# Performance work log

Measured on AMD Instinct MI355X. Metric: run time of the kernel, lower is better.

The kernel has to match this reference:

```python
import jax, jax.numpy as jnp
import numpy as np

N = 100000
E = 1600000
IN_DIM = 128
HID = 64
CLS = 10
L = 3
EPS = 1e-5


def setup_inputs() -> dict:
    key = jax.random.key(0)
    ks = jax.random.split(key, 12)
    x = jax.random.normal(ks[0], (N, IN_DIM), dtype=jnp.float32)
    edge_index = jax.random.randint(ks[1], (2, E), 0, N, dtype=jnp.int64)
    s = lambda k, shape, fan: jax.random.normal(k, shape, dtype=jnp.float32) / np.sqrt(fan)
    return {
        "x": x,
        "edge_index": edge_index,
        "fc1_w": s(ks[2], (HID, IN_DIM), IN_DIM),
        "fc1_b": jnp.zeros((HID,), jnp.float32),
        "lin_l_w": s(ks[3], (L, HID, HID), HID),   # neighbor (aggregated) weight, with bias
        "lin_l_b": jnp.zeros((L, HID), jnp.float32),
        "lin_r_w": s(ks[4], (L, HID, HID), HID),   # root/self weight, no bias (PyG SAGEConv)
        "bn_gamma": jnp.ones((L, HID), jnp.float32),
        "bn_beta": jnp.zeros((L, HID), jnp.float32),
        "fc2_w": s(ks[5], (CLS, HID), HID),
        "fc2_b": jnp.zeros((CLS,), jnp.float32),
    }


def reference(x, edge_index, fc1_w, fc1_b, lin_l_w, lin_l_b, lin_r_w,
              bn_gamma, bn_beta, fc2_w, fc2_b):
    src, dst = edge_index[0], edge_index[1]
    # in-degree counts for mean aggregation (zero-degree nodes -> 0 output)
    deg = jax.ops.segment_sum(jnp.ones((E,), x.dtype), dst, num_segments=N)
    inv_deg = jnp.where(deg > 0, 1.0 / jnp.maximum(deg, 1.0), 0.0)[:, None]

    h = jax.nn.relu(x @ fc1_w.T + fc1_b)  # [N, HID]
    for l in range(L):
        # SAGEConv: mean-aggregate neighbor features, then lin_l(agg) + lin_r(self)
        agg = jax.ops.segment_sum(h[src], dst, num_segments=N) * inv_deg  # [N, HID]
        h = agg @ lin_l_w[l].T + lin_l_b[l] + h @ lin_r_w[l].T
        # batch norm over node dimension (training batch statistics)
        mu = jnp.mean(h, axis=0)
        var = jnp.mean(jnp.square(h - mu), axis=0)
        h = (h - mu) * jax.lax.rsqrt(var + EPS) * bn_gamma[l] + bn_beta[l]
        h = jax.nn.relu(h)
    logits = h @ fc2_w.T + fc2_b  # [N, CLS]
    return jax.nn.log_softmax(logits, axis=1)
```

## Files before the change

kernel.cpp:

```cpp
#include <hip/hip_runtime.h>

#define N_NODES 100000
#define N_EDGES 1600000
#define IN_DIM  128
#define HID     64
#define CLS     10
#define NLAYER  3
#define BN_EPS  1e-5f
#define INV_N   (1.0f / N_NODES)
#define SREP    8
#define CAP     40
#define NW      32
#define WNODES  (N_NODES / NW)
#define PBLK    512
#define EPB     (N_EDGES / PBLK)
#define BCAP    152

typedef __attribute__((ext_vector_type(8))) short bf16x8;
typedef __attribute__((ext_vector_type(4))) float f32x4;
typedef __attribute__((ext_vector_type(2))) float f32x2;

__device__ __forceinline__ int clampi(int v, int lo, int hi) {
    return v < lo ? lo : (v > hi ? hi : v);
}

__device__ __forceinline__ unsigned bf16rne(float v) {
    unsigned u = __float_as_uint(v);
    return (u + 0x7fffu + ((u >> 16) & 1u)) >> 16;
}

__device__ __forceinline__ float bf2f(unsigned short u) {
    return __uint_as_float((unsigned)u << 16);
}

__device__ __forceinline__ void splitbf(float v, unsigned short& hi, unsigned short& lo) {
    unsigned h = bf16rne(v);
    hi = (unsigned short)h;
    lo = (unsigned short)bf16rne(v - __uint_as_float(h << 16));
}

#if defined(__has_builtin)
# if __has_builtin(__builtin_amdgcn_cvt_pk_f32_fp8) && __has_builtin(__builtin_amdgcn_cvt_pk_fp8_f32)
#  define HW_FP8 1
# endif
#endif
#ifndef HW_FP8
# define HW_FP8 0
#endif

__device__ __forceinline__ void fp8dec4(unsigned u, float* o) {
#if HW_FP8
    f32x2 lo = __builtin_amdgcn_cvt_pk_f32_fp8((int)u, false);
    f32x2 hi = __builtin_amdgcn_cvt_pk_f32_fp8((int)u, true);
    o[0] = lo[0]; o[1] = lo[1]; o[2] = hi[0]; o[3] = hi[1];
#else
#pragma unroll
    for (int k = 0; k < 4; k++) {
        unsigned b = (u >> (8 * k)) & 0xffu;
        unsigned s = b >> 7, e = (b >> 3) & 15u, m = b & 7u;
        float v = e ? __uint_as_float(((e + 120u) << 23) | (m << 20)) : (float)m * 0x1p-9f;
        o[k] = s ? -v : v;
    }
#endif
}

__device__ __forceinline__ unsigned fp8enc1(float v) {
#if HW_FP8
    return (unsigned)__builtin_amdgcn_cvt_pk_fp8_f32(v, 0.f, 0, false) & 0xffu;
#else
    float a = fabsf(v);
    unsigned s = __float_as_uint(v) >> 31;
    if (a > 448.f) a = 448.f;
    unsigned r;
    if (a < 0x1p-6f) {
        r = (unsigned)__float2int_rn(a * 512.f);
    } else {
        unsigned u = __float_as_uint(a);
        int ex = (int)(u >> 23) - 127;
        unsigned man = u & 0x7fffffu;
        unsigned mr = (man + 0x7ffffu + ((man >> 20) & 1u)) >> 20;
        if (mr == 8u) { mr = 0; ex++; }
        if (ex > 8) { ex = 8; mr = 7; }
        r = ((unsigned)(ex + 7) << 3) | mr;
    }
    return (s << 7) | r;
#endif
}

__device__ __forceinline__ float stat_sum(const float* __restrict__ s, int idx) {
    float a = 0.f;
#pragma unroll
    for (int r = 0; r < SREP; r++) a += s[r * 2 * HID + idx];
    return a;
}

__global__ __launch_bounds__(256) void k_bin(const int* __restrict__ ei,
                                             unsigned* __restrict__ binned,
                                             int* __restrict__ bcnt) {
    __shared__ int lcnt[NW];
    int t = threadIdx.x, b = blockIdx.x;
    if (t < NW) lcnt[t] = 0;
    __syncthreads();
    int e0 = b * EPB;
    int e1 = e0 + EPB; if (e1 > N_EDGES) e1 = N_EDGES;
    for (int e = e0 + t; e < e1; e += 256) {
        int d = clampi(ei[N_EDGES + e], 0, N_NODES - 1);
        int s = clampi(ei[e],           0, N_NODES - 1);
        int w  = d / WNODES;
        int dw = d - w * WNODES;
        int j = atomicAdd(&lcnt[w], 1);
        if (j < BCAP)
            binned[((size_t)w * PBLK + b) * BCAP + j] = ((unsigned)dw << 17) | (unsigned)s;
    }
    __syncthreads();
    if (t < NW) bcnt[t * PBLK + b] = lcnt[t] < BCAP ? lcnt[t] : BCAP;
}

__global__ __launch_bounds__(256) void k_scat2(const unsigned* __restrict__ binned,
                                               const int* __restrict__ bcnt,
                                               int* __restrict__ cursor,
                                               int* __restrict__ ssrc) {
    int w  = blockIdx.x >> 3;
    int jb = blockIdx.x & 7;
    int wv = threadIdx.x >> 6, ln = threadIdx.x & 63;
    for (int b = jb * 4 + wv; b < PBLK; b += 32) {
        int cnt = bcnt[w * PBLK + b];
        const unsigned* run = &binned[((size_t)w * PBLK + b) * BCAP];
        for (int i = ln; i < cnt; i += 64) {
            unsigned pk = run[i];
            int s  = (int)(pk & 0x1ffffu);
            int d  = w * WNODES + (int)(pk >> 17);
            int j = atomicAdd(&cursor[d], 1);
            if (j < CAP) ssrc[(size_t)d * CAP + j] = s;
        }
    }
}

__global__ void k_wprep(const float* __restrict__ lw, const float* __restrict__ rw,
                        short* __restrict__ whi, short* __restrict__ wlo) {
    int i = blockIdx.x * 256 + threadIdx.x;
    if (i >= NLAYER * 2 * HID * HID) return;
    int l   = i / (2 * HID * HID);
    int rem = i % (2 * HID * HID);
    int op  = rem / (HID * HID);
    int jk  = rem % (HID * HID);
    float w = (op == 0) ? lw[(size_t)l * HID * HID + jk] : rw[(size_t)l * HID * HID + jk];
    unsigned short h_, l_;
    splitbf(w, h_, l_);
    whi[i] = (short)h_;
    wlo[i] = (short)l_;
}

__global__ void k_wprep1(const float* __restrict__ w1,
                         short* __restrict__ w1hi, short* __restrict__ w1lo) {
    int i = blockIdx.x * 256 + threadIdx.x;
    if (i >= HID * IN_DIM) return;
    unsigned short h_, l_;
    splitbf(w1[i], h_, l_);
    w1hi[i] = (short)h_;
    w1lo[i] = (short)l_;
}

__global__ void k_wprep2(const float* __restrict__ w2,
                         short* __restrict__ w2hi, short* __restrict__ w2lo) {
    int i = blockIdx.x * 256 + threadIdx.x;
    if (i >= 16 * HID) return;
    int j = i >> 6, k = i & 63;
    float w = (j < CLS) ? w2[(size_t)j * HID + k] : 0.f;
    unsigned short h_, l_;
    splitbf(w, h_, l_);
    w2hi[i] = (short)h_;
    w2lo[i] = (short)l_;
}

__global__ __launch_bounds__(128) void k_fc1_mfma(const float* __restrict__ x,
                                                  const short* __restrict__ w1hi,
                                                  const short* __restrict__ w1lo,
                                                  const float* __restrict__ b,
                                                  short* __restrict__ hbf,
                                                  unsigned char* __restrict__ hf8) {
    int t = threadIdx.x;
    int lane = t & 63;
    int wv = t >> 6;
    int lr = lane & 15;
    int kg = lane >> 4;
    int n0 = (blockIdx.x * 2 + wv) * 16;

    f32x4 acc0 = {0.f,0.f,0.f,0.f}, acc1 = {0.f,0.f,0.f,0.f};
    f32x4 acc2 = {0.f,0.f,0.f,0.f}, acc3 = {0.f,0.f,0.f,0.f};

#pragma unroll
    for (int kh = 0; kh < 4; kh++) {
        int kb = kg * 8 + kh * 32;
        const float4 a01 = *(const float4*)&x[(size_t)(n0 + lr) * IN_DIM + kb];
        const float4 a23 = *(const float4*)&x[(size_t)(n0 + lr) * IN_DIM + kb + 4];
        float av[8] = {a01.x,a01.y,a01.z,a01.w,a23.x,a23.y,a23.z,a23.w};
        bf16x8 ah, al;
#pragma unroll
        for (int e = 0; e < 8; e++) {
            unsigned h1 = bf16rne(av[e]);
            ah[e] = (short)h1;
            al[e] = (short)bf16rne(av[e] - __uint_as_float(h1 << 16));
        }
#define JT1(JT_, ACC_) { \
        const bf16x8 fwh = *(const bf16x8*)&w1hi[(size_t)(JT_ * 16 + lr) * IN_DIM + kb]; \
        const bf16x8 fwl = *(const bf16x8*)&w1lo[(size_t)(JT_ * 16 + lr) * IN_DIM + kb]; \
        ACC_ = __builtin_amdgcn_mfma_f32_16x16x32_bf16(ah, fwh, ACC_, 0, 0, 0); \
        ACC_ = __builtin_amdgcn_mfma_f32_16x16x32_bf16(ah, fwl, ACC_, 0, 0, 0); \
        ACC_ = __builtin_amdgcn_mfma_f32_16x16x32_bf16(al, fwh, ACC_, 0, 0, 0); \
    }
        JT1(0, acc0) JT1(1, acc1) JT1(2, acc2) JT1(3, acc3)
#undef JT1
    }

    float bv0 = b[lr], bv1 = b[16 + lr], bv2 = b[32 + lr], bv3 = b[48 + lr];
#define EPI1(JT_, ACC_, BV_) { \
        _Pragma("unroll") \
        for (int r = 0; r < 4; r++) { \
            float v = fmaxf(ACC_[r] + BV_, 0.f); \
            size_t idx = (size_t)(n0 + kg * 4 + r) * HID + JT_ * 16 + lr; \
            hbf[idx] = (short)bf16rne(v); \
            hf8[idx] = (unsigned char)fp8enc1(v); \
        } \
    }
    EPI1(0, acc0, bv0) EPI1(1, acc1, bv1) EPI1(2, acc2, bv2) EPI1(3, acc3, bv3)
#undef EPI1
}

__global__ __launch_bounds__(256, 6) void k_agg(const unsigned char* __restrict__ act_f8,
                                                const int* __restrict__ cursor,
                                                const int* __restrict__ ssrc,
                                                short* __restrict__ agg_bf) {
    int wave = (blockIdx.x * 256 + threadIdx.x) >> 6;
    int lane = threadIdx.x & 63;
    int g  = lane >> 4;
    int gl = lane & 15;
    int n = wave;
    if (n >= N_NODES) return;

    int cnt = cursor[n];
    cnt = cnt < CAP ? cnt : CAP;
    int s = n * CAP;
    int e = s + cnt;
    float ax = 0.f, ay = 0.f, az = 0.f, aw = 0.f;
    int i = s + g;

#define ACCP(P_) do { \
        float v_[4]; \
        fp8dec4(P_, v_); \
        ax += v_[0]; ay += v_[1]; az += v_[2]; aw += v_[3]; \
    } while (0)

    for (; i + 12 < e; i += 16) {
        int u0 = ssrc[i], u1 = ssrc[i + 4], u2 = ssrc[i + 8], u3 = ssrc[i + 12];
        unsigned p0 = *(const unsigned*)&act_f8[(size_t)u0 * HID + gl * 4];
        unsigned p1 = *(const unsigned*)&act_f8[(size_t)u1 * HID + gl * 4];
        unsigned p2 = *(const unsigned*)&act_f8[(size_t)u2 * HID + gl * 4];
        unsigned p3 = *(const unsigned*)&act_f8[(size_t)u3 * HID + gl * 4];
        ACCP(p0); ACCP(p1); ACCP(p2); ACCP(p3);
    }
    for (; i < e; i += 4) {
        int u = ssrc[i];
        unsigned pv = *(const unsigned*)&act_f8[(size_t)u * HID + gl * 4];
        ACCP(pv);
    }
#undef ACCP

#pragma unroll
    for (int st = 16; st <= 32; st <<= 1) {
        ax += __shfl_xor(ax, st);
        ay += __shfl_xor(ay, st);
        az += __shfl_xor(az, st);
        aw += __shfl_xor(aw, st);
    }
    if (g == 0) {
        float id = (cnt > 0) ? 1.0f / (float)cnt : 0.f;
        ushort4 r;
        r.x = (unsigned short)bf16rne(ax * id);
        r.y = (unsigned short)bf16rne(ay * id);
        r.z = (unsigned short)bf16rne(az * id);
        r.w = (unsigned short)bf16rne(aw * id);
        *(ushort4*)&agg_bf[(size_t)n * HID + gl * 4] = r;
    }
}

__global__ __launch_bounds__(128) void k_gemm_mfma(
    short* __restrict__ agg,
    const short* __restrict__ hs,
    const float* __restrict__ scp, const float* __restrict__ shp, int use_bn,
    const short* __restrict__ wlhi, const short* __restrict__ wllo,
    const short* __restrict__ wrhi, const short* __restrict__ wrlo,
    const float* __restrict__ lb, float* __restrict__ stats_out)
{
    __shared__ float lstat[2 * HID];
    int t = threadIdx.x;
    for (int i = t; i < 2 * HID; i += 128) lstat[i] = 0.f;
    __syncthreads();
    int lane = t & 63;
    int wv = t >> 6;
    int lr = lane & 15;
    int kg = lane >> 4;
    int n0 = (blockIdx.x * 2 + wv) * 16;

    f32x4 acc0 = {0.f,0.f,0.f,0.f}, acc1 = {0.f,0.f,0.f,0.f};
    f32x4 acc2 = {0.f,0.f,0.f,0.f}, acc3 = {0.f,0.f,0.f,0.f};

#pragma unroll
    for (int kh = 0; kh < 2; kh++) {
        int kb = kg * 8 + kh * 32;
        bf16x8 ah = *(const bf16x8*)&agg[(size_t)(n0 + lr) * HID + kb];
        bf16x8 bh = *(const bf16x8*)&hs[(size_t)(n0 + lr) * HID + kb];
        if (use_bn) {
#pragma unroll
            for (int e = 0; e < 8; e++) {
                int c = kb + e;
                float v = fmaxf(bf2f((unsigned short)bh[e]) * scp[c] + shp[c], 0.f);
                bh[e] = (short)bf16rne(v);
            }
        }
#define JT(JT_, ACC_) { \
        const bf16x8 fwlh = *(const bf16x8*)&wlhi[(size_t)(JT_ * 16 + lr) * HID + kb]; \
        const bf16x8 fwll = *(const bf16x8*)&wllo[(size_t)(JT_ * 16 + lr) * HID + kb]; \
        const bf16x8 fwrh = *(const bf16x8*)&wrhi[(size_t)(JT_ * 16 + lr) * HID + kb]; \
        const bf16x8 fwrl = *(const bf16x8*)&wrlo[(size_t)(JT_ * 16 + lr) * HID + kb]; \
        ACC_ = __builtin_amdgcn_mfma_f32_16x16x32_bf16(ah, fwlh, ACC_, 0, 0, 0); \
        ACC_ = __builtin_amdgcn_mfma_f32_16x16x32_bf16(ah, fwll, ACC_, 0, 0, 0); \
        ACC_ = __builtin_amdgcn_mfma_f32_16x16x32_bf16(bh, fwrh, ACC_, 0, 0, 0); \
        ACC_ = __builtin_amdgcn_mfma_f32_16x16x32_bf16(bh, fwrl, ACC_, 0, 0, 0); \
    }
        JT(0, acc0) JT(1, acc1) JT(2, acc2) JT(3, acc3)
#undef JT
    }

    float lbv0 = lb[lr], lbv1 = lb[16 + lr], lbv2 = lb[32 + lr], lbv3 = lb[48 + lr];
#define EPI(JT_, ACC_, LBV_) { \
        float s_ = 0.f, q_ = 0.f; \
        _Pragma("unroll") \
        for (int r = 0; r < 4; r++) { \
            float v = ACC_[r] + LBV_; \
            size_t idx = (size_t)(n0 + kg * 4 + r) * HID + JT_ * 16 + lr; \
            agg[idx] = (short)bf16rne(v); \
            s_ += v; q_ += v * v; \
        } \
        s_ += __shfl_xor(s_, 16); s_ += __shfl_xor(s_, 32); \
        q_ += __shfl_xor(q_, 16); q_ += __shfl_xor(q_, 32); \
        if (kg == 0) { \
            atomicAdd(&lstat[JT_ * 16 + lr], s_); \
            atomicAdd(&lstat[HID + JT_ * 16 + lr], q_); \
        } \
    }
    EPI(0, acc0, lbv0) EPI(1, acc1, lbv1) EPI(2, acc2, lbv2) EPI(3, acc3, lbv3)
#undef EPI
    __syncthreads();
    int rep = blockIdx.x & (SREP - 1);
    for (int i = t; i < 2 * HID; i += 128)
        atomicAdd(&stats_out[rep * 2 * HID + i], lstat[i]);
}

__global__ __launch_bounds__(256) void k_bnact(const float* __restrict__ stats,
                                               const float* __restrict__ gamma,
                                               const float* __restrict__ beta,
                                               const short* __restrict__ pre_bf,
                                               unsigned char* __restrict__ act_f8,
                                               float* __restrict__ scO,
                                               float* __restrict__ shO) {
    __shared__ float lsc[HID], lsh[HID];
    int t = threadIdx.x;
    if (t < HID) {
        float mu  = stat_sum(stats, t) * INV_N;
        float var = stat_sum(stats, HID + t) * INV_N - mu * mu;
        float s = gamma[t] * rsqrtf(var + BN_EPS);
        lsc[t] = s;
        lsh[t] = beta[t] - mu * s;
        if (blockIdx.x == 0) { scO[t] = s; shO[t] = lsh[t]; }
    }
    __syncthreads();
    int gl = t & 15;
    float4 s4 = *(const float4*)&lsc[gl * 4];
    float4 h4 = *(const float4*)&lsh[gl * 4];
    size_t idx = (size_t)blockIdx.x * 256 + t;
    size_t total = (size_t)N_NODES * HID / 4;
    size_t stride = (size_t)gridDim.x * 256;
    for (; idx < total; idx += stride) {
        ushort4 v = ((const ushort4*)pre_bf)[idx];
        float f0 = fmaxf(bf2f(v.x) * s4.x + h4.x, 0.f);
        float f1 = fmaxf(bf2f(v.y) * s4.y + h4.y, 0.f);
        float f2 = fmaxf(bf2f(v.z) * s4.z + h4.z, 0.f);
        float f3 = fmaxf(bf2f(v.w) * s4.w + h4.w, 0.f);
        unsigned pk = fp8enc1(f0) | (fp8enc1(f1) << 8) | (fp8enc1(f2) << 16) | (fp8enc1(f3) << 24);
        ((unsigned*)act_f8)[idx] = pk;
    }
}

__global__ void k_bnprep(const float* __restrict__ stats,
                         const float* __restrict__ gamma,
                         const float* __restrict__ beta,
                         float* __restrict__ sc, float* __restrict__ sh) {
    int t = threadIdx.x;
    float mu  = stat_sum(stats, t) * INV_N;
    float var = stat_sum(stats, HID + t) * INV_N - mu * mu;
    float s = gamma[t] * rsqrtf(var + BN_EPS);
    sc[t] = s;
    sh[t] = beta[t] - mu * s;
}

__global__ __launch_bounds__(128) void k_fc2_mfma(const short* __restrict__ h_bf,
                                                  const float* __restrict__ scp,
                                                  const float* __restrict__ shp,
                                                  const short* __restrict__ w2hi,
                                                  const short* __restrict__ w2lo,
                                                  const float* __restrict__ b2,
                                                  float* __restrict__ out) {
    int t = threadIdx.x;
    int lane = t & 63;
    int wv = t >> 6;
    int lr = lane & 15;
    int kg = lane >> 4;
    int n0 = (blockIdx.x * 2 + wv) * 16;

    f32x4 acc = {0.f,0.f,0.f,0.f};
#pragma unroll
    for (int kh = 0; kh < 2; kh++) {
        int kb = kg * 8 + kh * 32;
        bf16x8 ah = *(const bf16x8*)&h_bf[(size_t)(n0 + lr) * HID + kb];
#pragma unroll
        for (int e = 0; e < 8; e++) {
            int c = kb + e;
            float v = fmaxf(bf2f((unsigned short)ah[e]) * scp[c] + shp[c], 0.f);
            ah[e] = (short)bf16rne(v);
        }
        const bf16x8 wh = *(const bf16x8*)&w2hi[(size_t)lr * HID + kb];
        const bf16x8 wl = *(const bf16x8*)&w2lo[(size_t)lr * HID + kb];
        acc = __builtin_amdgcn_mfma_f32_16x16x32_bf16(ah, wh, acc, 0, 0, 0);
        acc = __builtin_amdgcn_mfma_f32_16x16x32_bf16(ah, wl, acc, 0, 0, 0);
    }
    float b2v = (lr < CLS) ? b2[lr] : 0.f;
#pragma unroll
    for (int r = 0; r < 4; r++) {
        int row = n0 + kg * 4 + r;
        float v = (lr < CLS) ? (acc[r] + b2v) : -3.4e38f;
        float m = v;
#pragma unroll
        for (int o = 1; o < 16; o <<= 1) m = fmaxf(m, __shfl_xor(m, o));
        float ev = (lr < CLS) ? __expf(v - m) : 0.f;
        float se = ev;
#pragma unroll
        for (int o = 1; o < 16; o <<= 1) se += __shfl_xor(se, o);
        float lse = m + __logf(se);
        if (lr < CLS) out[(size_t)row * CLS + lr] = v - lse;
    }
}

extern "C" void kernel_launch(void* const* d_in, const int* in_sizes, int n_in,
                              void* d_out, int out_size, void* d_ws, size_t ws_size,
                              hipStream_t stream) {
    const float* x        = (const float*)d_in[0];
    const int*   ei       = (const int*)d_in[1];
    const float* fc1_w    = (const float*)d_in[2];
    const float* fc1_b    = (const float*)d_in[3];
    const float* lin_l_w  = (const float*)d_in[4];
    const float* lin_l_b  = (const float*)d_in[5];
    const float* lin_r_w  = (const float*)d_in[6];
    const float* bn_gamma = (const float*)d_in[7];
    const float* bn_beta  = (const float*)d_in[8];
    const float* fc2_w    = (const float*)d_in[9];
    const float* fc2_b    = (const float*)d_in[10];
    float* out = (float*)d_out;

    char* p = (char*)d_ws;
    short*         hA  = (short*)p;         p += (size_t)N_NODES * HID * 2;
    short*         hB  = (short*)p;         p += (size_t)N_NODES * HID * 2;
    unsigned char* f0  = (unsigned char*)p; p += (size_t)N_NODES * HID;
    char*  zbase   = p;
    int*   cursor  = (int*)p;   p += (size_t)N_NODES * 4;
    float* stats   = (float*)p; p += (size_t)NLAYER * SREP * 2 * HID * 4;
    size_t zbytes  = (size_t)(p - zbase);
    int*      ssrc   = (int*)p;      p += (size_t)N_NODES * CAP * 4;
    unsigned* binned = (unsigned*)p; p += (size_t)NW * PBLK * BCAP * 4;
    int*      bcnt   = (int*)p;      p += (size_t)NW * PBLK * 4;
    short* whi     = (short*)p; p += (size_t)NLAYER * 2 * HID * HID * 2;
    short* wlo     = (short*)p; p += (size_t)NLAYER * 2 * HID * HID * 2;
    short* w1hi    = (short*)p; p += (size_t)HID * IN_DIM * 2;
    short* w1lo    = (short*)p; p += (size_t)HID * IN_DIM * 2;
    short* w2hi    = (short*)p; p += (size_t)16 * HID * 2;
    short* w2lo    = (short*)p; p += (size_t)16 * HID * 2;
    float* scbuf   = (float*)p; p += (size_t)NLAYER * HID * 4;
    float* shbuf   = (float*)p; p += (size_t)NLAYER * HID * 4;

    hipMemsetAsync(zbase, 0, zbytes, stream);
    k_wprep  <<<(NLAYER * 2 * HID * HID + 255) / 256, 256, 0, stream>>>(lin_l_w, lin_r_w, whi, wlo);
    k_wprep1 <<<(HID * IN_DIM + 255) / 256, 256, 0, stream>>>(fc1_w, w1hi, w1lo);
    k_wprep2 <<<(16 * HID + 255) / 256, 256, 0, stream>>>(fc2_w, w2hi, w2lo);
    k_bin    <<<PBLK, 256, 0, stream>>>(ei, binned, bcnt);
    k_scat2  <<<NW * 8, 256, 0, stream>>>(binned, bcnt, cursor, ssrc);
    k_fc1_mfma<<<3125, 128, 0, stream>>>(x, w1hi, w1lo, fc1_b, hA, f0);

    const int AGG_GRID = (N_NODES + 3) / 4;

    short* hin = hA;
    short* buf = hB;
    for (int l = 0; l < NLAYER; l++) {
        int use_bn = (l > 0);
        const float* sc_in = scbuf + (size_t)(l > 0 ? l - 1 : 0) * HID;
        const float* sh_in = shbuf + (size_t)(l > 0 ? l - 1 : 0) * HID;
        k_agg<<<AGG_GRID, 256, 0, stream>>>(f0, cursor, ssrc, buf);
        k_gemm_mfma<<<3125, 128, 0, stream>>>(buf, hin,
                                              sc_in, sh_in, use_bn,
                                              whi + (size_t)(l * 2 + 0) * HID * HID,
                                              wlo + (size_t)(l * 2 + 0) * HID * HID,
                                              whi + (size_t)(l * 2 + 1) * HID * HID,
                                              wlo + (size_t)(l * 2 + 1) * HID * HID,
                                              lin_l_b + (size_t)l * HID,
                                              stats + (size_t)l * SREP * 2 * HID);
        if (l < NLAYER - 1) {
            k_bnact<<<1024, 256, 0, stream>>>(stats + (size_t)l * SREP * 2 * HID,
                                              bn_gamma + (size_t)l * HID,
                                              bn_beta + (size_t)l * HID,
                                              buf, f0,
                                              scbuf + (size_t)l * HID,
                                              shbuf + (size_t)l * HID);
        } else {
            k_bnprep<<<1, 64, 0, stream>>>(stats + (size_t)l * SREP * 2 * HID,
                                           bn_gamma + (size_t)l * HID,
                                           bn_beta + (size_t)l * HID,
                                           scbuf + (size_t)l * HID,
                                           shbuf + (size_t)l * HID);
        }
        short* th = hin; hin = buf; buf = th;
    }
    k_fc2_mfma<<<3125, 128, 0, stream>>>(hin, scbuf + (size_t)2 * HID, shbuf + (size_t)2 * HID,
                                         w2hi, w2lo, fc2_b, out);
}
```

Before: 371.9 us.

## Build per-node neighbor lists in LDS per bin and stream them out coalesced

The edge binning now uses 128 destination bins of 782 nodes each, and the per-bin scatter kernel runs one block per bin. Each block builds the neighbor slot lists and counts in shared memory with LDS atomics, then writes the finished ssrc region with int4 stores and sets cursor directly. This replaces global atomics and random global writes and drops the memset of cursor. The binned buffer now reuses the hB workspace. The costs are only 128 blocks with about 125KB of LDS each, which limits occupancy, and a smaller per-bin cap (64) that risks dropping edges when a bin overflows.

```diff
diff --git a/kernel.cpp b/kernel.cpp
--- a/kernel.cpp
+++ b/kernel.cpp
@@ -10,11 +10,11 @@
 #define INV_N   (1.0f / N_NODES)
 #define SREP    8
 #define CAP     40
-#define NW      32
-#define WNODES  (N_NODES / NW)
+#define NW      128
+#define WNODES  782
 #define PBLK    512
 #define EPB     (N_EDGES / PBLK)
-#define BCAP    152
+#define BCAP    64
 
 typedef __attribute__((ext_vector_type(8))) short bf16x8;
 typedef __attribute__((ext_vector_type(4))) float f32x4;
@@ -99,7 +99,7 @@
                                              int* __restrict__ bcnt) {
     __shared__ int lcnt[NW];
     int t = threadIdx.x, b = blockIdx.x;
-    if (t < NW) lcnt[t] = 0;
+    for (int i = t; i < NW; i += 256) lcnt[i] = 0;
     __syncthreads();
     int e0 = b * EPB;
     int e1 = e0 + EPB; if (e1 > N_EDGES) e1 = N_EDGES;
@@ -113,27 +113,45 @@
             binned[((size_t)w * PBLK + b) * BCAP + j] = ((unsigned)dw << 17) | (unsigned)s;
     }
     __syncthreads();
-    if (t < NW) bcnt[t * PBLK + b] = lcnt[t] < BCAP ? lcnt[t] : BCAP;
-}
-
-__global__ __launch_bounds__(256) void k_scat2(const unsigned* __restrict__ binned,
+    for (int i = t; i < NW; i += 256)
+        bcnt[i * PBLK + b] = lcnt[i] < BCAP ? lcnt[i] : BCAP;
+}
+
+__global__ __launch_bounds__(256) void k_scat3(const unsigned* __restrict__ binned,
                                                const int* __restrict__ bcnt,
                                                int* __restrict__ cursor,
                                                int* __restrict__ ssrc) {
-    int w  = blockIdx.x >> 3;
-    int jb = blockIdx.x & 7;
-    int wv = threadIdx.x >> 6, ln = threadIdx.x & 63;
-    for (int b = jb * 4 + wv; b < PBLK; b += 32) {
+    extern __shared__ int lds[];
+    int* slots = lds;
+    int* cnts  = lds + WNODES * CAP;
+    int w = blockIdx.x;
+    int t = threadIdx.x;
+    for (int i = t; i < WNODES; i += 256) cnts[i] = 0;
+    __syncthreads();
+    int wv = t >> 6, ln = t & 63;
+    for (int b = wv; b < PBLK; b += 4) {
         int cnt = bcnt[w * PBLK + b];
         const unsigned* run = &binned[((size_t)w * PBLK + b) * BCAP];
         for (int i = ln; i < cnt; i += 64) {
             unsigned pk = run[i];
             int s  = (int)(pk & 0x1ffffu);
-            int d  = w * WNODES + (int)(pk >> 17);
-            int j = atomicAdd(&cursor[d], 1);
-            if (j < CAP) ssrc[(size_t)d * CAP + j] = s;
+            int dw = (int)(pk >> 17);
+            int j = atomicAdd(&cnts[dw], 1);
+            if (j < CAP) slots[dw * CAP + j] = s;
         }
     }
+    __syncthreads();
+    int n0 = w * WNODES;
+    for (int i = t; i < WNODES; i += 256) {
+        int n = n0 + i;
+        if (n < N_NODES) cursor[n] = cnts[i] < CAP ? cnts[i] : CAP;
+    }
+    int limn = N_NODES - n0; if (limn > WNODES) limn = WNODES;
+    if (limn <= 0) return;
+    int lim4 = (limn * CAP) >> 2;
+    int4* dst = (int4*)&ssrc[(size_t)n0 * CAP];
+    const int4* src4 = (const int4*)slots;
+    for (int i = t; i < lim4; i += 256) dst[i] = src4[i];
 }
 
 __global__ void k_wprep(const float* __restrict__ lw, const float* __restrict__ rw,
@@ -471,13 +489,13 @@
     short*         hA  = (short*)p;         p += (size_t)N_NODES * HID * 2;
     short*         hB  = (short*)p;         p += (size_t)N_NODES * HID * 2;
     unsigned char* f0  = (unsigned char*)p; p += (size_t)N_NODES * HID;
+    unsigned* binned = (unsigned*)hB;
     char*  zbase   = p;
-    int*   cursor  = (int*)p;   p += (size_t)N_NODES * 4;
     float* stats   = (float*)p; p += (size_t)NLAYER * SREP * 2 * HID * 4;
     size_t zbytes  = (size_t)(p - zbase);
-    int*      ssrc   = (int*)p;      p += (size_t)N_NODES * CAP * 4;
-    unsigned* binned = (unsigned*)p; p += (size_t)NW * PBLK * BCAP * 4;
-    int*      bcnt   = (int*)p;      p += (size_t)NW * PBLK * 4;
+    int*   cursor  = (int*)p;   p += (size_t)N_NODES * 4;
+    int*   ssrc    = (int*)p;   p += (size_t)N_NODES * CAP * 4;
+    int*   bcnt    = (int*)p;   p += (size_t)NW * PBLK * 4;
     short* whi     = (short*)p; p += (size_t)NLAYER * 2 * HID * HID * 2;
     short* wlo     = (short*)p; p += (size_t)NLAYER * 2 * HID * HID * 2;
     short* w1hi    = (short*)p; p += (size_t)HID * IN_DIM * 2;
@@ -492,7 +510,8 @@
     k_wprep1 <<<(HID * IN_DIM + 255) / 256, 256, 0, stream>>>(fc1_w, w1hi, w1lo);
     k_wprep2 <<<(16 * HID + 255) / 256, 256, 0, stream>>>(fc2_w, w2hi, w2lo);
     k_bin    <<<PBLK, 256, 0, stream>>>(ei, binned, bcnt);
-    k_scat2  <<<NW * 8, 256, 0, stream>>>(binned, bcnt, cursor, ssrc);
+    const int SCAT_LDS = (WNODES * CAP + WNODES) * 4;
+    k_scat3  <<<NW, 256, SCAT_LDS, stream>>>(binned, bcnt, cursor, ssrc);
     k_fc1_mfma<<<3125, 128, 0, stream>>>(x, w1hi, w1lo, fc1_b, hA, f0);
 
     const int AGG_GRID = (N_NODES + 3) / 4;
```

After: 382.9 us. 3.0% more time.
